# Optimization experiments

Measured on AMD Instinct MI355X. Metric: run time of the kernel, lower is better.

The kernel has to match this reference:

```python
import jax, jax.numpy as jnp
import numpy as np

B, N, D, H = 4, 4096, 256, 8
HD = D // H
EPS = 1e-09


def _feature_map(t):
    # ELU(x) + 1, strictly positive feature map (Katharopoulos et al. 2020)
    return jax.nn.elu(t) + 1.0


def setup_inputs() -> dict:
    key = jax.random.key(0)
    ks = jax.random.split(key, 8)
    s = 0.02  # weight init scale for numerical stability
    return {
        "x": jax.random.normal(ks[0], (B, N, D), dtype=jnp.float32),
        "prior": jax.random.normal(ks[1], (B, N, N), dtype=jnp.float32),
        "Wq": jax.random.normal(ks[2], (D, D), dtype=jnp.float32) * s,
        "Wk": jax.random.normal(ks[3], (D, D), dtype=jnp.float32) * s,
        "Wv": jax.random.normal(ks[4], (D, D), dtype=jnp.float32) * s,
        "bv": jax.random.normal(ks[5], (D,), dtype=jnp.float32) * s,
        "Wo": jax.random.normal(ks[6], (D, D), dtype=jnp.float32) * s,
        "bo": jax.random.normal(ks[7], (D,), dtype=jnp.float32) * s,
    }


def reference(x, prior, Wq, Wk, Wv, bv, Wo, bo):
    b, n, d = x.shape
    # bias: mean over last axis of prior -> (b, n, 1, 1), broadcast over heads/dims
    bias = jnp.mean(prior, axis=-1)[:, :, None, None]
    q = _feature_map(jnp.einsum("bnd,ed->bne", x, Wq).reshape(b, n, H, HD) + bias)
    padding_mask = jnp.all(q == 0, axis=-1)  # (b, n, H)
    k = _feature_map(jnp.einsum("bnd,ed->bne", x, Wk).reshape(b, n, H, HD))
    v = _feature_map((jnp.einsum("bnd,ed->bne", x, Wv) + bv).reshape(b, n, H, HD))
    # KV summary state: (b, h, m, d) with m = value dim, d = key feature dim
    kv = jnp.einsum("bnhd,bnhm->bhmd", k, v)
    # normalizer: q . sum_n(k)
    z = 1.0 / (jnp.einsum("bnhd,bhd->bnh", q, jnp.sum(k, axis=1)) + EPS)
    attn = jnp.einsum("bnhd,bhmd,bnh->bnhm", q, kv, z)
    attn = jnp.where(padding_mask[..., None], 0.0, attn)
    attn = attn.reshape(b, n, H * HD)
    return jnp.einsum("bnd,ed->bne", attn, Wo) + bo
```

## Files before the change

### kernel.cpp

```cpp
#include <hip/hip_runtime.h>
#include <hip/hip_bf16.h>
#include <math.h>

#define B_ 4
#define N_ 4096
#define D_ 256
#define H_ 8
#define HD_ 32
#define TOKENS (B_ * N_)
#define EPSF 1e-9f

typedef __bf16 bf16x8 __attribute__((ext_vector_type(8)));
typedef float f32x4 __attribute__((ext_vector_type(4)));
typedef ushort ushort8_t __attribute__((ext_vector_type(8)));

__device__ __forceinline__ float elu1(float x) { return x > 0.f ? x + 1.f : __expf(x); }

__device__ __forceinline__ ushort f2bf(float f) {
    __hip_bfloat16 h = __float2bfloat16(f);
    return *reinterpret_cast<ushort*>(&h);
}

#define GLOAD_LDS16(g, l)                                                              \
    __builtin_amdgcn_global_load_lds((__attribute__((address_space(1))) const void*)(g), \
                                     (__attribute__((address_space(3))) void*)(l), 16, 0, 0)

#define MFMA16(a, b, c) __builtin_amdgcn_mfma_f32_16x16x32_bf16((a), (b), (c), 0, 0, 0)

__global__ __launch_bounds__(256) void k_cvt_w(const float* __restrict__ Wq,
                                               const float* __restrict__ Wk,
                                               const float* __restrict__ Wv,
                                               const float* __restrict__ Wo,
                                               ushort* __restrict__ dst,
                                               float4* __restrict__ zbuf) {
    const int i = blockIdx.x * 256 + threadIdx.x;
    if (i < 8448) zbuf[i] = float4{0.f, 0.f, 0.f, 0.f};
    const int sel = i >> 13;
    const float* src = sel == 0 ? Wq : sel == 1 ? Wk : sel == 2 ? Wv : Wo;
    const int j = i & 8191;
    const float4* s = (const float4*)src + (size_t)j * 2;
    const float4 a = s[0], b = s[1];
    ushort8_t o;
    o[0] = f2bf(a.x); o[1] = f2bf(a.y); o[2] = f2bf(a.z); o[3] = f2bf(a.w);
    o[4] = f2bf(b.x); o[5] = f2bf(b.y); o[6] = f2bf(b.z); o[7] = f2bf(b.w);
    *((ushort8_t*)dst + i) = o;
}

__global__ __launch_bounds__(512, 2) void k_mix2(const float* __restrict__ prior,
                                                 const float* __restrict__ x,
                                                 const ushort* __restrict__ wq,
                                                 const ushort* __restrict__ wk,
                                                 const ushort* __restrict__ wv,
                                                 const float* __restrict__ bv,
                                                 float* __restrict__ bias_g,
                                                 ushort* __restrict__ qpre,
                                                 ushort* __restrict__ kb,
                                                 ushort* __restrict__ vb) {
    __shared__ ushort As[32 * 256];
    __shared__ ushort Ws[3 * 256 * 32];
    const int t = threadIdx.x;
    const int w = t >> 6, lane = t & 63;
    const int bid = blockIdx.x;

    if (bid % 5 != 0) {
        const int bidx = bid - bid / 5 - 1;
        const int row = bidx * 8 + w;
        const f32x4* p = (const f32x4*)(prior + (size_t)row * N_);
        float s0 = 0.f, s1 = 0.f, s2 = 0.f, s3 = 0.f;
#pragma unroll
        for (int i = 0; i < 4; ++i) {
            const f32x4 a = __builtin_nontemporal_load(p + (i * 4 + 0) * 64 + lane);
            const f32x4 b = __builtin_nontemporal_load(p + (i * 4 + 1) * 64 + lane);
            const f32x4 c = __builtin_nontemporal_load(p + (i * 4 + 2) * 64 + lane);
            const f32x4 d = __builtin_nontemporal_load(p + (i * 4 + 3) * 64 + lane);
            s0 += a[0] + a[1] + a[2] + a[3];
            s1 += b[0] + b[1] + b[2] + b[3];
            s2 += c[0] + c[1] + c[2] + c[3];
            s3 += d[0] + d[1] + d[2] + d[3];
        }
        float s = (s0 + s1) + (s2 + s3);
#pragma unroll
        for (int off = 32; off; off >>= 1) s += __shfl_xor(s, off, 64);
        if (lane == 0) bias_g[row] = s * (1.0f / N_);
        return;
    }

    const int rowBase = (bid / 5) * 32;

    {
        const int r = t >> 4;
        const int c0 = (t & 15) * 4;
#pragma unroll
        for (int j = 0; j < 4; ++j) {
            const int c = c0 + j * 64;
            const float4 xv = *(const float4*)(x + (size_t)(rowBase + r) * 256 + c);
            ushort4 o;
            o.x = f2bf(xv.x); o.y = f2bf(xv.y); o.z = f2bf(xv.z); o.w = f2bf(xv.w);
            const int byte = (r * 512 + c * 2) ^ ((r & 7) << 4);
            *(ushort4*)((char*)As + byte) = o;
        }
    }

    const int wr = w >> 2, wc = w & 3;
    const int q_ = lane >> 4;
    f32x4 accq[4] = {}, acck[4] = {}, accv[4] = {};

    for (int kt = 0; kt < 256; kt += 32) {
        __syncthreads();
#pragma unroll
        for (int j = 0; j < 6; ++j) {
            const int c = j * 512 + t;
            const int idx = c & 1023;
            const int e = idx >> 2;
            const int pslot = idx & 3;
            const int qsrc = pslot ^ ((e >> 1) & 3);
            const ushort* srcm = (j < 2) ? wq : (j < 4) ? wk : wv;
            GLOAD_LDS16(srcm + (size_t)e * 256 + kt + qsrc * 8, (char*)Ws + c * 16);
        }
        __syncthreads();
        const int r = wr * 16 + (lane & 15);
        const int abyte = (r * 512 + (kt + q_ * 8) * 2) ^ ((r & 7) << 4);
        const bf16x8 af = *(const bf16x8*)((const char*)As + abyte);
#pragma unroll
        for (int n = 0; n < 4; ++n) {
            const int e = wc * 64 + n * 16 + (lane & 15);
            const int wbyte = e * 64 + ((q_ ^ ((e >> 1) & 3)) * 16);
            const bf16x8 bq = *(const bf16x8*)((const char*)Ws + wbyte);
            const bf16x8 bk = *(const bf16x8*)((const char*)Ws + 16384 + wbyte);
            const bf16x8 bw = *(const bf16x8*)((const char*)Ws + 32768 + wbyte);
            accq[n] = MFMA16(af, bq, accq[n]);
            acck[n] = MFMA16(af, bk, acck[n]);
            accv[n] = MFMA16(af, bw, accv[n]);
        }
    }

#pragma unroll
    for (int n = 0; n < 4; ++n)
#pragma unroll
        for (int j = 0; j < 4; ++j) {
            const int rl = wr * 16 + (lane >> 4) * 4 + j;
            const int col = wc * 64 + n * 16 + (lane & 15);
            const size_t go = (size_t)(rowBase + rl) * 256 + col;
            qpre[go] = f2bf(accq[n][j]);
            kb[go]   = f2bf(elu1(acck[n][j]));
            vb[go]   = f2bf(elu1(accv[n][j] + bv[col]));
        }
}

__global__ __launch_bounds__(256) void k_kvsum(const ushort* __restrict__ kmat,
                                               const ushort* __restrict__ vmat,
                                               float* __restrict__ kv,
                                               float* __restrict__ ksum) {
    const int bh = blockIdx.x;
    const int b = bh >> 3, h = bh & 7;
    const int CH = gridDim.y;
    const int rows = N_ / CH;
    const int tok0 = b * N_ + blockIdx.y * rows;
    __shared__ float kt_[64][32];
    __shared__ float vt_[64][32];
    const int t = threadIdx.x;
    const int m = t >> 3;
    const int lvec = (t & 7) * 4;
    float4 acc = {0.f, 0.f, 0.f, 0.f};
    float4 sk = {0.f, 0.f, 0.f, 0.f};
    for (int r0 = 0; r0 < rows; r0 += 64) {
        __syncthreads();
#pragma unroll
        for (int half = 0; half < 2; ++half) {
            const int rr = (t >> 3) + half * 32;
            const size_t g = (size_t)(tok0 + r0 + rr) * D_ + h * HD_ + lvec;
            const ushort4 ku = *(const ushort4*)(kmat + g);
            const ushort4 vu = *(const ushort4*)(vmat + g);
            kt_[rr][lvec + 0] = __bfloat162float(*(const __hip_bfloat16*)&ku.x);
            kt_[rr][lvec + 1] = __bfloat162float(*(const __hip_bfloat16*)&ku.y);
            kt_[rr][lvec + 2] = __bfloat162float(*(const __hip_bfloat16*)&ku.z);
            kt_[rr][lvec + 3] = __bfloat162float(*(const __hip_bfloat16*)&ku.w);
            vt_[rr][lvec + 0] = __bfloat162float(*(const __hip_bfloat16*)&vu.x);
            vt_[rr][lvec + 1] = __bfloat162float(*(const __hip_bfloat16*)&vu.y);
            vt_[rr][lvec + 2] = __bfloat162float(*(const __hip_bfloat16*)&vu.z);
            vt_[rr][lvec + 3] = __bfloat162float(*(const __hip_bfloat16*)&vu.w);
        }
        __syncthreads();
#pragma unroll 4
        for (int r = 0; r < 64; ++r) {
            const float vv = vt_[r][m];
            const float4 kk = *(const float4*)&kt_[r][lvec];
            acc.x = fmaf(vv, kk.x, acc.x);
            acc.y = fmaf(vv, kk.y, acc.y);
            acc.z = fmaf(vv, kk.z, acc.z);
            acc.w = fmaf(vv, kk.w, acc.w);
            sk.x += kk.x; sk.y += kk.y; sk.z += kk.z; sk.w += kk.w;
        }
    }
    float* kvp = kv + ((size_t)bh * HD_ + m) * HD_ + lvec;
    atomicAdd(kvp + 0, acc.x);
    atomicAdd(kvp + 1, acc.y);
    atomicAdd(kvp + 2, acc.z);
    atomicAdd(kvp + 3, acc.w);
    if (m == 0) {
        float* kp = ksum + (size_t)bh * HD_ + lvec;
        atomicAdd(kp + 0, sk.x);
        atomicAdd(kp + 1, sk.y);
        atomicAdd(kp + 2, sk.z);
        atomicAdd(kp + 3, sk.w);
    }
}

__global__ __launch_bounds__(512, 2) void k_fusedB(const ushort* __restrict__ qpre,
                                                   const float* __restrict__ bias_g,
                                                   const float* __restrict__ kv,
                                                   const float* __restrict__ ksum,
                                                   const ushort* __restrict__ wo,
                                                   const float* __restrict__ bo,
                                                   float* __restrict__ out) {
    __shared__ ushort qs[64 * 256];
    __shared__ ushort at_s[64 * 256];
    __shared__ ushort Ws2[256 * 32];
    const int t = threadIdx.x;
    const int w = t >> 6, lane = t & 63;
    const int tokBase = blockIdx.x * 64;
    const int b = tokBase >> 12;

#pragma unroll
    for (int j = 0; j < 4; ++j) {
        const int chunk = j * 512 + t;
        GLOAD_LDS16(qpre + (size_t)tokBase * 256 + (size_t)chunk * 8,
                    (char*)qs + chunk * 16);
    }

    const int c = t & 255;
    const int h = c >> 5, m = c & 31;
    f32x4 kvr[8], ksr[8];
#pragma unroll
    for (int i = 0; i < 8; ++i) {
        kvr[i] = *(const f32x4*)(kv + (((size_t)(b * H_ + h) * HD_ + m) * HD_) + i * 4);
        ksr[i] = *(const f32x4*)(ksum + (size_t)(b * H_ + h) * HD_ + i * 4);
    }
    __syncthreads();

    {
        const int r = t >> 3;
        const float brow = bias_g[tokBase + r];
        const int cb = (t & 7) * 32;
#pragma unroll
        for (int i = 0; i < 4; ++i) {
            bf16x8 qv = *(bf16x8*)(qs + r * 256 + cb + i * 8);
#pragma unroll
            for (int j = 0; j < 8; ++j) qv[j] = (__bf16)elu1((float)qv[j] + brow);
            *(bf16x8*)(qs + r * 256 + cb + i * 8) = qv;
        }
    }
    __syncthreads();

    for (int tok2 = 0; tok2 < 32; ++tok2) {
        const int tok = tok2 * 2 + (t >> 8);
        float num = 0.f, den = 0.f;
#pragma unroll
        for (int i = 0; i < 4; ++i) {
            const bf16x8 qv = *(const bf16x8*)(qs + tok * 256 + h * HD_ + i * 8);
#pragma unroll
            for (int j = 0; j < 8; ++j) {
                const float qf = (float)qv[j];
                num = fmaf(qf, ((const float*)kvr)[i * 8 + j], num);
                den = fmaf(qf, ((const float*)ksr)[i * 8 + j], den);
            }
        }
        const float a = num / (den + EPSF);
        const int byte = (tok * 512 + c * 2) ^ ((tok & 7) << 4);
        *(ushort*)((char*)at_s + byte) = f2bf(a);
    }

    const int wr = w >> 2, wc = w & 3;
    const int q_ = lane >> 4;
    f32x4 acc[2][4] = {};
    for (int kt = 0; kt < 256; kt += 32) {
        __syncthreads();
#pragma unroll
        for (int j = 0; j < 2; ++j) {
            const int ch = j * 512 + t;
            const int e = ch >> 2;
            const int pslot = ch & 3;
            const int qsrc = pslot ^ ((e >> 1) & 3);
            GLOAD_LDS16(wo + (size_t)e * 256 + kt + qsrc * 8, (char*)Ws2 + ch * 16);
        }
        __syncthreads();
        bf16x8 af[2];
#pragma unroll
        for (int mm = 0; mm < 2; ++mm) {
            const int r = wr * 32 + mm * 16 + (lane & 15);
            const int byte = (r * 512 + (kt + q_ * 8) * 2) ^ ((r & 7) << 4);
            af[mm] = *(const bf16x8*)((const char*)at_s + byte);
        }
#pragma unroll
        for (int n = 0; n < 4; ++n) {
            const int e = wc * 64 + n * 16 + (lane & 15);
            const int wbyte = e * 64 + ((q_ ^ ((e >> 1) & 3)) * 16);
            const bf16x8 bw = *(const bf16x8*)((const char*)Ws2 + wbyte);
#pragma unroll
            for (int mm = 0; mm < 2; ++mm)
                acc[mm][n] = MFMA16(af[mm], bw, acc[mm][n]);
        }
    }
#pragma unroll
    for (int mm = 0; mm < 2; ++mm)
#pragma unroll
        for (int n = 0; n < 4; ++n)
#pragma unroll
            for (int j = 0; j < 4; ++j) {
                const int row = tokBase + wr * 32 + mm * 16 + (lane >> 4) * 4 + j;
                const int col = wc * 64 + n * 16 + (lane & 15);
                out[(size_t)row * 256 + col] = acc[mm][n][j] + bo[col];
            }
}

extern "C" void kernel_launch(void* const* d_in, const int* in_sizes, int n_in,
                              void* d_out, int out_size, void* d_ws, size_t ws_size,
                              hipStream_t stream) {
    const float* x     = (const float*)d_in[0];
    const float* prior = (const float*)d_in[1];
    const float* Wq    = (const float*)d_in[2];
    const float* Wk    = (const float*)d_in[3];
    const float* Wv    = (const float*)d_in[4];
    const float* bv    = (const float*)d_in[5];
    const float* Wo    = (const float*)d_in[6];
    const float* bo    = (const float*)d_in[7];
    float* out = (float*)d_out;

    char* w8 = (char*)d_ws;
    ushort* qpre = (ushort*)w8;
    ushort* kb   = qpre + (size_t)TOKENS * D_;
    ushort* vb   = kb + (size_t)TOKENS * D_;
    ushort* wqb  = vb + (size_t)TOKENS * D_;
    ushort* wkb  = wqb + 65536;
    ushort* wvb  = wkb + 65536;
    ushort* wob  = wvb + 65536;
    float* kvb   = (float*)(wqb + 4 * 65536);
    float* ksb   = kvb + 32768;
    float* bias  = ksb + 1024;

    k_cvt_w<<<128, 256, 0, stream>>>(Wq, Wk, Wv, Wo, wqb, (float4*)kvb);

    k_mix2<<<2560, 512, 0, stream>>>(prior, x, wqb, wkb, wvb, bv, bias, qpre, kb, vb);

    k_kvsum<<<dim3(32, 8), 256, 0, stream>>>(kb, vb, kvb, ksb);

    k_fusedB<<<256, 512, 0, stream>>>(qpre, bias, kvb, ksb, wob, bo, out);
}
```

Before: 109.5 us.

## Double GEMM row tile per block and split kv reduction into more chunks

The QKV projection part of the mixed kernel now handles 64 rows per block instead of 32. Each wave computes two 16-row MFMA tiles, so every weight tile staged in LDS is reused twice and fewer blocks reload the weights. The GEMM blocks are placed first and the prior-mean blocks after them, replacing the old 1-in-5 interleave. The kv summary kernel is split into 32 chunks per head instead of 8 for more parallelism. The tradeoffs are more LDS and accumulator registers per block, which may reduce occupancy, and more atomic or partial accumulation traffic in k_kvsum.

```diff
diff --git a/kernel.cpp b/kernel.cpp
--- a/kernel.cpp
+++ b/kernel.cpp
@@ -46,7 +46,7 @@
     *((ushort8_t*)dst + i) = o;
 }
 
-__global__ __launch_bounds__(512, 2) void k_mix2(const float* __restrict__ prior,
+__global__ __launch_bounds__(512, 2) void k_mix4(const float* __restrict__ prior,
                                                  const float* __restrict__ x,
                                                  const ushort* __restrict__ wq,
                                                  const ushort* __restrict__ wk,
@@ -56,15 +56,14 @@
                                                  ushort* __restrict__ qpre,
                                                  ushort* __restrict__ kb,
                                                  ushort* __restrict__ vb) {
-    __shared__ ushort As[32 * 256];
+    __shared__ ushort As[64 * 256];
     __shared__ ushort Ws[3 * 256 * 32];
     const int t = threadIdx.x;
     const int w = t >> 6, lane = t & 63;
     const int bid = blockIdx.x;
 
-    if (bid % 5 != 0) {
-        const int bidx = bid - bid / 5 - 1;
-        const int row = bidx * 8 + w;
+    if (bid >= 256) {
+        const int row = (bid - 256) * 8 + w;
         const f32x4* p = (const f32x4*)(prior + (size_t)row * N_);
         float s0 = 0.f, s1 = 0.f, s2 = 0.f, s3 = 0.f;
 #pragma unroll
@@ -85,14 +84,14 @@
         return;
     }
 
-    const int rowBase = (bid / 5) * 32;
+    const int rowBase = bid * 64;
 
     {
-        const int r = t >> 4;
-        const int c0 = (t & 15) * 4;
-#pragma unroll
-        for (int j = 0; j < 4; ++j) {
-            const int c = c0 + j * 64;
+        const int r = t >> 3;
+        const int c0 = (t & 7) * 4;
+#pragma unroll
+        for (int j = 0; j < 8; ++j) {
+            const int c = c0 + j * 32;
             const float4 xv = *(const float4*)(x + (size_t)(rowBase + r) * 256 + c);
             ushort4 o;
             o.x = f2bf(xv.x); o.y = f2bf(xv.y); o.z = f2bf(xv.z); o.w = f2bf(xv.w);
@@ -103,7 +102,7 @@
 
     const int wr = w >> 2, wc = w & 3;
     const int q_ = lane >> 4;
-    f32x4 accq[4] = {}, acck[4] = {}, accv[4] = {};
+    f32x4 accq[2][4] = {}, acck[2][4] = {}, accv[2][4] = {};
 
     for (int kt = 0; kt < 256; kt += 32) {
         __syncthreads();
@@ -118,9 +117,13 @@
             GLOAD_LDS16(srcm + (size_t)e * 256 + kt + qsrc * 8, (char*)Ws + c * 16);
         }
         __syncthreads();
-        const int r = wr * 16 + (lane & 15);
-        const int abyte = (r * 512 + (kt + q_ * 8) * 2) ^ ((r & 7) << 4);
-        const bf16x8 af = *(const bf16x8*)((const char*)As + abyte);
+        bf16x8 af[2];
+#pragma unroll
+        for (int mm = 0; mm < 2; ++mm) {
+            const int r = wr * 32 + mm * 16 + (lane & 15);
+            const int abyte = (r * 512 + (kt + q_ * 8) * 2) ^ ((r & 7) << 4);
+            af[mm] = *(const bf16x8*)((const char*)As + abyte);
+        }
 #pragma unroll
         for (int n = 0; n < 4; ++n) {
             const int e = wc * 64 + n * 16 + (lane & 15);
@@ -128,23 +131,28 @@
             const bf16x8 bq = *(const bf16x8*)((const char*)Ws + wbyte);
             const bf16x8 bk = *(const bf16x8*)((const char*)Ws + 16384 + wbyte);
             const bf16x8 bw = *(const bf16x8*)((const char*)Ws + 32768 + wbyte);
-            accq[n] = MFMA16(af, bq, accq[n]);
-            acck[n] = MFMA16(af, bk, acck[n]);
-            accv[n] = MFMA16(af, bw, accv[n]);
-        }
-    }
-
-#pragma unroll
-    for (int n = 0; n < 4; ++n)
-#pragma unroll
-        for (int j = 0; j < 4; ++j) {
-            const int rl = wr * 16 + (lane >> 4) * 4 + j;
-            const int col = wc * 64 + n * 16 + (lane & 15);
-            const size_t go = (size_t)(rowBase + rl) * 256 + col;
-            qpre[go] = f2bf(accq[n][j]);
-            kb[go]   = f2bf(elu1(acck[n][j]));
-            vb[go]   = f2bf(elu1(accv[n][j] + bv[col]));
-        }
+#pragma unroll
+            for (int mm = 0; mm < 2; ++mm) {
+                accq[mm][n] = MFMA16(af[mm], bq, accq[mm][n]);
+                acck[mm][n] = MFMA16(af[mm], bk, acck[mm][n]);
+                accv[mm][n] = MFMA16(af[mm], bw, accv[mm][n]);
+            }
+        }
+    }
+
+#pragma unroll
+    for (int mm = 0; mm < 2; ++mm)
+#pragma unroll
+        for (int n = 0; n < 4; ++n)
+#pragma unroll
+            for (int j = 0; j < 4; ++j) {
+                const int rl = wr * 32 + mm * 16 + (lane >> 4) * 4 + j;
+                const int col = wc * 64 + n * 16 + (lane & 15);
+                const size_t go = (size_t)(rowBase + rl) * 256 + col;
+                qpre[go] = f2bf(accq[mm][n][j]);
+                kb[go]   = f2bf(elu1(acck[mm][n][j]));
+                vb[go]   = f2bf(elu1(accv[mm][n][j] + bv[col]));
+            }
 }
 
 __global__ __launch_bounds__(256) void k_kvsum(const ushort* __restrict__ kmat,
@@ -340,9 +348,9 @@
 
     k_cvt_w<<<128, 256, 0, stream>>>(Wq, Wk, Wv, Wo, wqb, (float4*)kvb);
 
-    k_mix2<<<2560, 512, 0, stream>>>(prior, x, wqb, wkb, wvb, bv, bias, qpre, kb, vb);
-
-    k_kvsum<<<dim3(32, 8), 256, 0, stream>>>(kb, vb, kvb, ksb);
+    k_mix4<<<2304, 512, 0, stream>>>(prior, x, wqb, wkb, wvb, bv, bias, qpre, kb, vb);
+
+    k_kvsum<<<dim3(32, 32), 256, 0, stream>>>(kb, vb, kvb, ksb);
 
     k_fusedB<<<256, 512, 0, stream>>>(qpre, bias, kvb, ksb, wob, bo, out);
 }
```

New measurement: 126.8 us. 1.16x slower.
